# Kernel optimization log

Measured on AMD Instinct MI355X. Metric: run time of the kernel, lower is better.

Reference implementation:

```python
import jax, jax.numpy as jnp
import numpy as np

N_NODES = 50000
D = 128
E_RAND = 640000
ALPHA = 0.2  # LeakyReLU negative slope


def setup_inputs() -> dict:
    key = jax.random.key(0)
    k1, k2, k3, k4, k5 = jax.random.split(key, 5)
    inputs = jax.random.normal(k1, (N_NODES, D), dtype=jnp.float32) * 0.1
    # xavier_normal with gain=1.414 as in the torch module
    W = jax.random.normal(k2, (D, D), dtype=jnp.float32) * (1.414 * np.sqrt(2.0 / (D + D)))
    a = jax.random.normal(k3, (2 * D,), dtype=jnp.float32) * (1.414 * np.sqrt(2.0 / (1 + 2 * D)))
    # random edges + self-loops so every node has at least one outgoing edge (nonzero rowsum)
    src = jnp.concatenate([jax.random.randint(k4, (E_RAND,), 0, N_NODES), jnp.arange(N_NODES)])
    dst = jnp.concatenate([jax.random.randint(k5, (E_RAND,), 0, N_NODES), jnp.arange(N_NODES)])
    edge = jnp.stack([src, dst]).astype(jnp.int64)
    return {"inputs": inputs, "edge": edge, "W": W, "a": a}


def reference(inputs, edge, W, a):
    N = inputs.shape[0]
    src, dst = edge[0], edge[1]
    h = inputs @ W  # [N, D]
    # a @ [h_src; h_dst] per edge == h_src @ a[:D] + h_dst @ a[D:]
    score = h[src] @ a[:D] + h[dst] @ a[D:]  # [E]
    edge_e = jnp.exp(jax.nn.leaky_relu(score, negative_slope=ALPHA))  # [E]
    # sparse.mm(coo(edge, edge_e), ones): rowsum over src (coalesce sums duplicates)
    e_rowsum = jax.ops.segment_sum(edge_e, src, num_segments=N)  # [N]
    # sparse.mm(coo(edge, edge_e), h): weighted aggregation of h[dst] into src rows
    h_prime = jax.ops.segment_sum(edge_e[:, None] * h[dst], src, num_segments=N)  # [N, D]
    h_prime = h_prime / e_rowsum[:, None]
    return jax.nn.elu(h_prime)
```

## Files before the change

### kernel.cpp

```cpp
#include <hip/hip_runtime.h>
#include <hip/hip_bf16.h>


constexpr int D   = 128;
constexpr int CH  = 8192;
constexpr int CAP = 4608;

typedef __attribute__((ext_vector_type(8))) short bf16x8;
typedef __attribute__((ext_vector_type(4))) float f32x4;

__device__ __forceinline__ short f2bf(float f) {
    unsigned u = __float_as_uint(f);
    unsigned r = (u + 0x7fffu + ((u >> 16) & 1u)) >> 16;
    return (short)r;
}
__device__ __forceinline__ float bf2f(short b) {
    return __uint_as_float(((unsigned)(unsigned short)b) << 16);
}
__device__ __forceinline__ short2 pk_bf16(float x, float y) {
    __hip_bfloat162 bb = __float22bfloat162_rn(make_float2(x, y));
    short2 r;
    __builtin_memcpy(&r, &bb, 4);
    return r;
}

__global__ __launch_bounds__(256) void sort_and_gemm(
    const float* __restrict__ X, const float* __restrict__ W,
    const float* __restrict__ a,
    const int* __restrict__ src, const int* __restrict__ dst,
    int* __restrict__ bucket_cnt, int* __restrict__ binned,
    short* __restrict__ h, float* __restrict__ s1, float* __restrict__ s2,
    int NBK, int NC, int N, int E) {
    __shared__ short lbw[2048 * 8];
    if (blockIdx.x < (unsigned)NC) {
        int* hist = (int*)lbw;
        int* base = hist + 256;
        const int c = blockIdx.x, t = threadIdx.x;
        hist[t] = 0;
        __syncthreads();
        const int lo = c * CH, hi = min(lo + CH, E);
        const int hi4 = lo + ((hi - lo) & ~3);
        for (int i = lo + t * 4; i < hi4; i += 1024) {
            const int4 s4 = *(const int4*)(src + i);
            atomicAdd(&hist[s4.x >> 8], 1);
            atomicAdd(&hist[s4.y >> 8], 1);
            atomicAdd(&hist[s4.z >> 8], 1);
            atomicAdd(&hist[s4.w >> 8], 1);
        }
        for (int i = hi4 + t; i < hi; i += 256)
            atomicAdd(&hist[src[i] >> 8], 1);
        __syncthreads();
        if (t < NBK) base[t] = atomicAdd(&bucket_cnt[t], hist[t]);
        hist[t] = 0;
        __syncthreads();
        for (int i = lo + t * 4; i < hi4; i += 1024) {
            const int4 s4 = *(const int4*)(src + i);
            const int4 d4 = *(const int4*)(dst + i);
            const int sv[4] = {s4.x, s4.y, s4.z, s4.w};
            const int dv[4] = {d4.x, d4.y, d4.z, d4.w};
#pragma unroll
            for (int j = 0; j < 4; ++j) {
                const int b = sv[j] >> 8;
                const int r = atomicAdd(&hist[b], 1);
                binned[b * CAP + base[b] + r] = ((sv[j] & 255) << 16) | dv[j];
            }
        }
        for (int i = hi4 + t; i < hi; i += 256) {
            const int s = src[i];
            const int b = s >> 8;
            const int r = atomicAdd(&hist[b], 1);
            binned[b * CAP + base[b] + r] = ((s & 255) << 16) | dst[i];
        }
        return;
    }
    for (int i = threadIdx.x; i < 2048; i += 256) {
        const int l = i & 63, st = i >> 6;
        const int s = st >> 3, tt = st & 7;
        const int n = tt * 16 + (l & 15);
        const int q = l >> 4;
#pragma unroll
        for (int j = 0; j < 8; ++j)
            lbw[i * 8 + j] = f2bf(W[(s * 32 + q * 8 + j) * D + n]);
    }
    __syncthreads();

    const int wave = threadIdx.x >> 6, lane = threadIdx.x & 63;
    const int r0 = (blockIdx.x - NC) * 64 + wave * 16;
    const int m = lane & 15, q = lane >> 4;
    const int arow = r0 + m;
    const bool rowok = arow < N;
    const float* xp = X + (size_t)arow * D + q * 8;

    f32x4 acc[8] = {};
#pragma unroll
    for (int s = 0; s < 4; ++s) {
        float4 xa = {0, 0, 0, 0}, xb = {0, 0, 0, 0};
        if (rowok) {
            xa = *(const float4*)(xp + s * 32);
            xb = *(const float4*)(xp + s * 32 + 4);
        }
        bf16x8 af;
        short2 c0 = pk_bf16(xa.x, xa.y), c1 = pk_bf16(xa.z, xa.w);
        short2 c2 = pk_bf16(xb.x, xb.y), c3 = pk_bf16(xb.z, xb.w);
        af[0] = c0.x; af[1] = c0.y; af[2] = c1.x; af[3] = c1.y;
        af[4] = c2.x; af[5] = c2.y; af[6] = c3.x; af[7] = c3.y;
#pragma unroll
        for (int t = 0; t < 8; ++t) {
            bf16x8 bf = *(const bf16x8*)(lbw + ((s * 8 + t) * 64 + lane) * 8);
            acc[t] = __builtin_amdgcn_mfma_f32_16x16x32_bf16(af, bf, acc[t], 0, 0, 0);
        }
    }
    float a1v[8], a2v[8];
#pragma unroll
    for (int t = 0; t < 8; ++t) {
        a1v[t] = a[t * 16 + m];
        a2v[t] = a[D + t * 16 + m];
    }
    float p1[4] = {0, 0, 0, 0}, p2[4] = {0, 0, 0, 0};
#pragma unroll
    for (int t = 0; t < 8; ++t) {
        short2 h01 = pk_bf16(acc[t][0], acc[t][1]);
        short2 h23 = pk_bf16(acc[t][2], acc[t][3]);
        const short hb[4] = {h01.x, h01.y, h23.x, h23.y};
#pragma unroll
        for (int i = 0; i < 4; ++i) {
            const int row = r0 + q * 4 + i;
            if (row < N) h[(size_t)row * D + t * 16 + m] = hb[i];
            const float hr = bf2f(hb[i]);
            p1[i] += hr * a1v[t];
            p2[i] += hr * a2v[t];
        }
    }
#pragma unroll
    for (int off = 1; off < 16; off <<= 1) {
#pragma unroll
        for (int i = 0; i < 4; ++i) {
            p1[i] += __shfl_xor(p1[i], off);
            p2[i] += __shfl_xor(p2[i], off);
        }
    }
    if (m < 4) {
        const int row = r0 + q * 4 + m;
        if (row < N) {
            const float v1 = (m == 0) ? p1[0] : (m == 1) ? p1[1] : (m == 2) ? p1[2] : p1[3];
            const float v2 = (m == 0) ? p2[0] : (m == 1) ? p2[1] : (m == 2) ? p2[2] : p2[3];
            s1[row] = v1;
            s2[row] = v2;
        }
    }
}

__global__ __launch_bounds__(256) void fine_scatter(
    const int* __restrict__ binned, const int* __restrict__ bucket_cnt,
    int2* __restrict__ bounds, int* __restrict__ csrd, int N) {
    __shared__ int ncnt[256], snc[256], exclp[256], pcnt[256];
    const int b = blockIdx.x, t = threadIdx.x;
    ncnt[t] = 0;
    pcnt[t] = 0;
    __syncthreads();
    const int start = b * CAP;
    const int end = start + bucket_cnt[b];
    for (int i = start + t; i < end; i += 256)
        atomicAdd(&ncnt[binned[i] >> 16], 1);
    __syncthreads();
    snc[t] = ncnt[t];
    __syncthreads();
    for (int off = 1; off < 256; off <<= 1) {
        int v = (t >= off) ? snc[t - off] : 0;
        __syncthreads();
        snc[t] += v;
        __syncthreads();
    }
    exclp[t] = snc[t] - ncnt[t];
    const int node = b * 256 + t;
    if (node < N) bounds[node] = make_int2(start + exclp[t], start + exclp[t] + ncnt[t]);
    __syncthreads();
    for (int i = start + t; i < end; i += 256) {
        const int e = binned[i];
        const int r = e >> 16;
        csrd[start + exclp[r] + atomicAdd(&pcnt[r], 1)] = e & 0xFFFF;
    }
}

__global__ __launch_bounds__(256) void aggregate(
    const int* __restrict__ csrd, const int2* __restrict__ bounds,
    const float* __restrict__ s1, const float* __restrict__ s2,
    const short* __restrict__ h, float* __restrict__ out, int N) {
    const int n    = blockIdx.x * 4 + (threadIdx.x >> 6);
    const int lane = threadIdx.x & 63;
    if (n >= N) return;
    const int g = lane >> 4, m = lane & 15;
    const int2 be = bounds[n];
    const int beg = be.x, end = be.y;
    const float s1n = s1[n];

    int dA1 = csrd[min(beg + g, end - 1)];
    int dB1 = csrd[min(beg + 4 + g, end - 1)];
    float  sA0 = s2[dA1], sB0 = s2[dB1];
    bf16x8 rA0 = *(const bf16x8*)(h + (size_t)dA1 * D + m * 8);
    bf16x8 rB0 = *(const bf16x8*)(h + (size_t)dB1 * D + m * 8);
    dA1 = csrd[min(beg + 8 + g, end - 1)];
    dB1 = csrd[min(beg + 12 + g, end - 1)];

    float acc[8] = {};
    float rs = 0.f;
    for (int k0 = beg; k0 < end; k0 += 8) {
        const float  sA1 = s2[dA1];
        const float  sB1 = s2[dB1];
        const bf16x8 rA1 = *(const bf16x8*)(h + (size_t)dA1 * D + m * 8);
        const bf16x8 rB1 = *(const bf16x8*)(h + (size_t)dB1 * D + m * 8);
        dA1 = csrd[min(k0 + 16 + g, end - 1)];
        dB1 = csrd[min(k0 + 20 + g, end - 1)];

        float scA = s1n + sA0;
        scA = scA > 0.f ? scA : 0.2f * scA;
        float eA = __expf(scA);
        if (k0 + g >= end) eA = 0.f;
        float scB = s1n + sB0;
        scB = scB > 0.f ? scB : 0.2f * scB;
        float eB = __expf(scB);
        if (k0 + 4 + g >= end) eB = 0.f;
#pragma unroll
        for (int j = 0; j < 8; ++j)
            acc[j] += eA * bf2f(rA0[j]) + eB * bf2f(rB0[j]);
        rs += eA + eB;
        sA0 = sA1; sB0 = sB1; rA0 = rA1; rB0 = rB1;
    }
#pragma unroll
    for (int off = 16; off <= 32; off <<= 1) {
        rs += __shfl_xor(rs, off);
#pragma unroll
        for (int j = 0; j < 8; ++j) acc[j] += __shfl_xor(acc[j], off);
    }
    if (g == 0) {
        const float inv = 1.f / rs;
        float o[8];
#pragma unroll
        for (int j = 0; j < 8; ++j) {
            float v = acc[j] * inv;
            o[j] = v > 0.f ? v : expm1f(v);
        }
        float* op = out + (size_t)n * D + m * 8;
        *(float4*)op       = make_float4(o[0], o[1], o[2], o[3]);
        *(float4*)(op + 4) = make_float4(o[4], o[5], o[6], o[7]);
    }
}

extern "C" void kernel_launch(void* const* d_in, const int* in_sizes, int n_in,
                              void* d_out, int out_size, void* d_ws, size_t ws_size,
                              hipStream_t stream) {
    const float* X    = (const float*)d_in[0];
    const int*   edge = (const int*)d_in[1];
    const float* W    = (const float*)d_in[2];
    const float* a    = (const float*)d_in[3];
    float* out = (float*)d_out;

    const int N = in_sizes[0] / D;
    const int E = in_sizes[1] / 2;
    const int* src = edge;
    const int* dst = edge + E;

    const int NBK = (N + 255) >> 8;
    const int NC  = (E + CH - 1) / CH;
    const int NG  = (N + 63) / 64;

    char* ws = (char*)d_ws;
    short* h        = (short*)ws; ws += (size_t)N * D * sizeof(short);
    int* binned     = (int*)ws;   ws += (size_t)NBK * CAP * sizeof(int);
    int* csrd       = (int*)ws;   ws += (size_t)NBK * CAP * sizeof(int);
    float* s1       = (float*)ws; ws += (size_t)N * sizeof(float);
    float* s2       = (float*)ws; ws += (size_t)N * sizeof(float);
    int2* bounds    = (int2*)ws;  ws += (size_t)N * sizeof(int2);
    int* bucket_cnt = (int*)ws;   ws += 256 * sizeof(int);

    (void)hipMemsetAsync(bucket_cnt, 0, NBK * sizeof(int), stream);
    sort_and_gemm<<<NC + NG, 256, 0, stream>>>(X, W, a, src, dst, bucket_cnt,
                                               binned, h, s1, s2, NBK, NC, N, E);
    fine_scatter<<<NBK, 256, 0, stream>>>(binned, bucket_cnt, bounds, csrd, N);
    aggregate<<<(N + 3) / 4, 256, 0, stream>>>(csrd, bounds, s1, s2, h, out, N);
}
```

Baseline: 140.8 us.

## Precompute bf16 W fragments in an init kernel, drop memset, and guard aggregate prefetch

```diff
diff --git a/kernel.cpp b/kernel.cpp
--- a/kernel.cpp
+++ b/kernel.cpp
@@ -24,17 +24,34 @@
     return r;
 }
 
+__global__ __launch_bounds__(256) void init(const float* __restrict__ W,
+                                            short* __restrict__ bw,
+                                            int* __restrict__ bucket_cnt, int NBK) {
+    if (blockIdx.x == 8) {
+        if (threadIdx.x < NBK) bucket_cnt[threadIdx.x] = 0;
+        return;
+    }
+    const int tid = blockIdx.x * 256 + threadIdx.x;
+    const int l = tid & 63, st = tid >> 6;
+    const int s = st >> 3, t = st & 7;
+    const int n = t * 16 + (l & 15);
+    const int q = l >> 4;
+#pragma unroll
+    for (int j = 0; j < 8; ++j) {
+        const int k = s * 32 + q * 8 + j;
+        bw[tid * 8 + j] = f2bf(W[k * D + n]);
+    }
+}
+
 __global__ __launch_bounds__(256) void sort_and_gemm(
-    const float* __restrict__ X, const float* __restrict__ W,
+    const float* __restrict__ X, const short* __restrict__ bw,
     const float* __restrict__ a,
     const int* __restrict__ src, const int* __restrict__ dst,
     int* __restrict__ bucket_cnt, int* __restrict__ binned,
     short* __restrict__ h, float* __restrict__ s1, float* __restrict__ s2,
     int NBK, int NC, int N, int E) {
-    __shared__ short lbw[2048 * 8];
+    __shared__ int hist[256], base[256];
     if (blockIdx.x < (unsigned)NC) {
-        int* hist = (int*)lbw;
-        int* base = hist + 256;
         const int c = blockIdx.x, t = threadIdx.x;
         hist[t] = 0;
         __syncthreads();
@@ -73,17 +90,6 @@
         }
         return;
     }
-    for (int i = threadIdx.x; i < 2048; i += 256) {
-        const int l = i & 63, st = i >> 6;
-        const int s = st >> 3, tt = st & 7;
-        const int n = tt * 16 + (l & 15);
-        const int q = l >> 4;
-#pragma unroll
-        for (int j = 0; j < 8; ++j)
-            lbw[i * 8 + j] = f2bf(W[(s * 32 + q * 8 + j) * D + n]);
-    }
-    __syncthreads();
-
     const int wave = threadIdx.x >> 6, lane = threadIdx.x & 63;
     const int r0 = (blockIdx.x - NC) * 64 + wave * 16;
     const int m = lane & 15, q = lane >> 4;
@@ -106,7 +112,7 @@
         af[4] = c2.x; af[5] = c2.y; af[6] = c3.x; af[7] = c3.y;
 #pragma unroll
         for (int t = 0; t < 8; ++t) {
-            bf16x8 bf = *(const bf16x8*)(lbw + ((s * 8 + t) * 64 + lane) * 8);
+            bf16x8 bf = *(const bf16x8*)(bw + ((s * 8 + t) * 64 + lane) * 8);
             acc[t] = __builtin_amdgcn_mfma_f32_16x16x32_bf16(af, bf, acc[t], 0, 0, 0);
         }
     }
@@ -194,24 +200,31 @@
     const int beg = be.x, end = be.y;
     const float s1n = s1[n];
 
-    int dA1 = csrd[min(beg + g, end - 1)];
-    int dB1 = csrd[min(beg + 4 + g, end - 1)];
-    float  sA0 = s2[dA1], sB0 = s2[dB1];
-    bf16x8 rA0 = *(const bf16x8*)(h + (size_t)dA1 * D + m * 8);
-    bf16x8 rB0 = *(const bf16x8*)(h + (size_t)dB1 * D + m * 8);
-    dA1 = csrd[min(beg + 8 + g, end - 1)];
-    dB1 = csrd[min(beg + 12 + g, end - 1)];
+    int dA0 = csrd[min(beg + g, end - 1)];
+    int dB0 = csrd[min(beg + 4 + g, end - 1)];
+    float  sA0 = s2[dA0], sB0 = s2[dB0];
+    bf16x8 rA0 = *(const bf16x8*)(h + (size_t)dA0 * D + m * 8);
+    bf16x8 rB0 = *(const bf16x8*)(h + (size_t)dB0 * D + m * 8);
+    int dA1 = 0, dB1 = 0;
+    if (beg + 8 < end) {
+        dA1 = csrd[min(beg + 8 + g, end - 1)];
+        dB1 = csrd[min(beg + 12 + g, end - 1)];
+    }
 
     float acc[8] = {};
     float rs = 0.f;
     for (int k0 = beg; k0 < end; k0 += 8) {
-        const float  sA1 = s2[dA1];
-        const float  sB1 = s2[dB1];
-        const bf16x8 rA1 = *(const bf16x8*)(h + (size_t)dA1 * D + m * 8);
-        const bf16x8 rB1 = *(const bf16x8*)(h + (size_t)dB1 * D + m * 8);
-        dA1 = csrd[min(k0 + 16 + g, end - 1)];
-        dB1 = csrd[min(k0 + 20 + g, end - 1)];
-
+        const bool more = (k0 + 8) < end;
+        float sA1, sB1;
+        bf16x8 rA1, rB1;
+        if (more) {
+            sA1 = s2[dA1];
+            sB1 = s2[dB1];
+            rA1 = *(const bf16x8*)(h + (size_t)dA1 * D + m * 8);
+            rB1 = *(const bf16x8*)(h + (size_t)dB1 * D + m * 8);
+            dA1 = csrd[min(k0 + 16 + g, end - 1)];
+            dB1 = csrd[min(k0 + 20 + g, end - 1)];
+        }
         float scA = s1n + sA0;
         scA = scA > 0.f ? scA : 0.2f * scA;
         float eA = __expf(scA);
@@ -224,7 +237,7 @@
         for (int j = 0; j < 8; ++j)
             acc[j] += eA * bf2f(rA0[j]) + eB * bf2f(rB0[j]);
         rs += eA + eB;
-        sA0 = sA1; sB0 = sB1; rA0 = rA1; rB0 = rB1;
+        if (more) { sA0 = sA1; sB0 = sB1; rA0 = rA1; rB0 = rB1; }
     }
 #pragma unroll
     for (int off = 16; off <= 32; off <<= 1) {
@@ -268,13 +281,14 @@
     short* h        = (short*)ws; ws += (size_t)N * D * sizeof(short);
     int* binned     = (int*)ws;   ws += (size_t)NBK * CAP * sizeof(int);
     int* csrd       = (int*)ws;   ws += (size_t)NBK * CAP * sizeof(int);
+    short* bw       = (short*)ws; ws += 2048 * 8 * sizeof(short);
     float* s1       = (float*)ws; ws += (size_t)N * sizeof(float);
     float* s2       = (float*)ws; ws += (size_t)N * sizeof(float);
     int2* bounds    = (int2*)ws;  ws += (size_t)N * sizeof(int2);
     int* bucket_cnt = (int*)ws;   ws += 256 * sizeof(int);
 
-    (void)hipMemsetAsync(bucket_cnt, 0, NBK * sizeof(int), stream);
-    sort_and_gemm<<<NC + NG, 256, 0, stream>>>(X, W, a, src, dst, bucket_cnt,
+    init<<<9, 256, 0, stream>>>(W, bw, bucket_cnt, NBK);
+    sort_and_gemm<<<NC + NG, 256, 0, stream>>>(X, bw, a, src, dst, bucket_cnt,
                                                binned, h, s1, s2, NBK, NC, N, E);
     fine_scatter<<<NBK, 256, 0, stream>>>(binned, bucket_cnt, bounds, csrd, N);
     aggregate<<<(N + 3) / 4, 256, 0, stream>>>(csrd, bounds, s1, s2, h, out, N);
```

After: 139.3 us. About the same (-1.1%).
